# Kernel optimization log

Measured on AMD Instinct MI355X. Metric: run time of the kernel, lower is better.

## Reference

```python
import jax, jax.numpy as jnp
import numpy as np

LMBDA = 0.01
GAMMA = 0.5  # resolvant_gamma


def get_mask(evals_x, evals_y, gamma):
    # Standard DPFM resolvant mask, vectorized over batch.
    # evals_x, evals_y: [B, K] nonnegative eigenvalues.
    scale = jnp.maximum(evals_x.max(-1), evals_y.max(-1))[:, None]  # per-batch scaling
    e1 = (evals_x / scale) ** gamma  # [B, K] -> columns of D
    e2 = (evals_y / scale) ** gamma  # [B, K] -> rows of D
    denom = e1[:, None, :] ** 2 + e2[:, :, None] ** 2  # [B, K, K]
    M_re = (e2[:, :, None] - e1[:, None, :]) / denom
    M_im = 1.0 / denom
    return M_re ** 2 + M_im ** 2  # [B, K, K]


def setup_inputs() -> dict:
    key = jax.random.key(0)
    kA, kB, kx, ky = jax.random.split(key, 4)
    Bsz, K, C = 8, 200, 352
    A = jax.random.normal(kA, (Bsz, K, C), dtype=jnp.float32)
    B = jax.random.normal(kB, (Bsz, K, C), dtype=jnp.float32)
    evals_x = jax.random.uniform(kx, (Bsz, K), dtype=jnp.float32)
    evals_y = jax.random.uniform(ky, (Bsz, K), dtype=jnp.float32)
    return {"A": A, "B": B, "evals_x": evals_x, "evals_y": evals_y}


def reference(A, B, evals_x, evals_y):
    # A, B: [Bsz, K, C]; evals_*: [Bsz, K]
    D = get_mask(evals_x, evals_y, GAMMA)  # [Bsz, K, K]
    A_t = jnp.swapaxes(A, 1, 2)            # [Bsz, C, K]
    A_A_t = jnp.matmul(A, A_t)             # [Bsz, K, K]
    B_A_t = jnp.matmul(B, A_t)             # [Bsz, K, K]
    K = A.shape[1]
    eye = jnp.eye(K, dtype=A.dtype)
    # mats[b, i] = A_A_t[b] + lmbda * diag(D[b, i, :])  -> [Bsz, K, K, K]
    mats = A_A_t[:, None, :, :] + LMBDA * (D[..., None] * eye)
    rhs = B_A_t[..., None]                 # [Bsz, K, K, 1] (row i of B_A_t as column)
    # Solve each regularized system; rows of Cxy are the solutions.
    Cxy = jnp.linalg.solve(mats, rhs)[..., 0]  # [Bsz, K, K]
    return Cxy
```

## Files before the change

kernel.cpp:

```cpp
#include <hip/hip_runtime.h>
#include <math.h>

#define KD 200
#define CD 352
#define NITER 28
#define LMB 0.01f

__device__ __forceinline__ float4 ld4(const float* p) { return *(const float4*)p; }
__device__ __forceinline__ void st4(float* p, float4 v) { *(float4*)p = v; }
__device__ __forceinline__ float rdlane(float v, int lane) {
    return __int_as_float(__builtin_amdgcn_readlane(__float_as_int(v), lane));
}

__global__ __launch_bounds__(256) void gemm_gr_kernel(
    const float* __restrict__ A, const float* __restrict__ B,
    float* __restrict__ G, float* __restrict__ R)
{
    __shared__ __align__(16) float Ms[16][72];
    __shared__ __align__(16) float Ns[16][72];
    const int tid = threadIdx.x;
    const int z = blockIdx.z;
    const int b = z >> 1, which = z & 1;
    const float* __restrict__ Xb = (which ? B : A) + (size_t)b * KD * CD;
    const float* __restrict__ Ab = A + (size_t)b * KD * CD;
    float* __restrict__ O = (which ? R : G) + (size_t)b * KD * KD;
    const int tileM = blockIdx.y * 64;
    const int tileN = blockIdx.x * 64;

    const int lm = tid >> 2;
    const int kq = (tid & 3) * 4;
    const int rowM = min(tileM + lm, KD - 1);
    const int rowN = min(tileN + lm, KD - 1);
    const float* __restrict__ Xrow = Xb + (size_t)rowM * CD;
    const float* __restrict__ Arow = Ab + (size_t)rowN * CD;

    const int ty = tid >> 4, tx = tid & 15;
    const int m0 = ty * 4, n0 = tx * 4;

    float acc[4][4] = {};
    for (int kk = 0; kk < CD; kk += 16) {
        const float4 vx = ld4(Xrow + kk + kq);
        const float4 va = ld4(Arow + kk + kq);
        __syncthreads();
        Ms[kq + 0][lm] = vx.x; Ms[kq + 1][lm] = vx.y;
        Ms[kq + 2][lm] = vx.z; Ms[kq + 3][lm] = vx.w;
        Ns[kq + 0][lm] = va.x; Ns[kq + 1][lm] = va.y;
        Ns[kq + 2][lm] = va.z; Ns[kq + 3][lm] = va.w;
        __syncthreads();
        #pragma unroll
        for (int k = 0; k < 16; ++k) {
            const float4 am = ld4(&Ms[k][m0]);
            const float4 an = ld4(&Ns[k][n0]);
            acc[0][0] = fmaf(am.x, an.x, acc[0][0]);
            acc[0][1] = fmaf(am.x, an.y, acc[0][1]);
            acc[0][2] = fmaf(am.x, an.z, acc[0][2]);
            acc[0][3] = fmaf(am.x, an.w, acc[0][3]);
            acc[1][0] = fmaf(am.y, an.x, acc[1][0]);
            acc[1][1] = fmaf(am.y, an.y, acc[1][1]);
            acc[1][2] = fmaf(am.y, an.z, acc[1][2]);
            acc[1][3] = fmaf(am.y, an.w, acc[1][3]);
            acc[2][0] = fmaf(am.z, an.x, acc[2][0]);
            acc[2][1] = fmaf(am.z, an.y, acc[2][1]);
            acc[2][2] = fmaf(am.z, an.z, acc[2][2]);
            acc[2][3] = fmaf(am.z, an.w, acc[2][3]);
            acc[3][0] = fmaf(am.w, an.x, acc[3][0]);
            acc[3][1] = fmaf(am.w, an.y, acc[3][1]);
            acc[3][2] = fmaf(am.w, an.z, acc[3][2]);
            acc[3][3] = fmaf(am.w, an.w, acc[3][3]);
        }
    }
    const int gn = tileN + n0;
    if (gn < KD) {
        #pragma unroll
        for (int i = 0; i < 4; ++i) {
            const int gm = tileM + m0 + i;
            if (gm < KD)
                st4(&O[(size_t)gm * KD + gn],
                    make_float4(acc[i][0], acc[i][1], acc[i][2], acc[i][3]));
        }
    }
}

__global__ __launch_bounds__(512) void cg_kernel(
    const float* __restrict__ G, const float* __restrict__ R,
    const float* __restrict__ ex, const float* __restrict__ ey,
    float* __restrict__ out)
{
    __shared__ __align__(16) float P[KD * 8];
    __shared__ __align__(16) float PART[8 * KD * 8];
    __shared__ float WP1[8][8];
    __shared__ float WP2[8][8];
    __shared__ float red8[8];

    const int tid = threadIdx.x;
    const int w = tid >> 6, l = tid & 63;
    const int blk = blockIdx.x;
    const int b = blk / 25;
    const int i0 = (blk - b * 25) * 8;
    const int bK = b * KD;
    const float* __restrict__ Gb = G + (size_t)b * KD * KD;

    float mxv = 0.f;
    if (tid < KD) mxv = fmaxf(ex[bK + tid], ey[bK + tid]);
    #pragma unroll
    for (int off = 32; off > 0; off >>= 1)
        mxv = fmaxf(mxv, __shfl_down(mxv, off, 64));
    if (l == 0) red8[w] = mxv;
    __syncthreads();
    float scale = red8[0];
    #pragma unroll
    for (int wv = 1; wv < 8; ++wv) scale = fmaxf(scale, red8[wv]);
    const float inv_scale = 1.0f / scale;

    const bool mact = (l < 50);
    const int gcol = mact ? l : 49;

    float4 g0[8];
    {
        const float* __restrict__ gp = Gb + (size_t)(w * 8) * KD + gcol;
        #pragma unroll
        for (int dc = 0; dc < 8; ++dc) {
            g0[dc] = make_float4(gp[0], gp[50], gp[100], gp[150]);
            gp += KD;
        }
    }

    const bool stid = tid < 400;
    const int r = tid >> 1, sq = tid & 1;
    float lam[4], dinv[4], rr[4], xx[4], pp[4], rz4[4];
    if (stid) {
        const float exj = ex[bK + r] * inv_scale;
        const float e1 = sqrtf(exj);
        const float gdiag = Gb[(size_t)r * KD + r];
        const float* __restrict__ Rb = R + (size_t)(bK + i0 + sq * 4) * KD + r;
        #pragma unroll
        for (int j = 0; j < 4; ++j) {
            const float eyi = ey[bK + i0 + sq * 4 + j] * inv_scale;
            const float e2 = sqrtf(eyi);
            const float dn = exj + eyi;
            const float re = e2 - e1;
            lam[j] = LMB * ((re * re + 1.f) / (dn * dn));
            dinv[j] = 1.f / (gdiag + lam[j]);
            rr[j] = Rb[(size_t)j * KD];
            pp[j] = rr[j] * dinv[j];
            xx[j] = 0.f;
        }
        st4(&P[r * 8 + sq * 4], make_float4(pp[0], pp[1], pp[2], pp[3]));
    }
    {
        float vg[4];
        #pragma unroll
        for (int j = 0; j < 4; ++j) vg[j] = stid ? rr[j] * pp[j] : 0.f;
        #pragma unroll
        for (int off = 2; off < 64; off <<= 1)
            #pragma unroll
            for (int j = 0; j < 4; ++j) vg[j] += __shfl_xor(vg[j], off, 64);
        if (l < 2) {
            #pragma unroll
            for (int j = 0; j < 4; ++j) WP1[w][l * 4 + j] = vg[j];
        }
    }
    __syncthreads();
    if (stid) {
        #pragma unroll
        for (int j = 0; j < 4; ++j) {
            float s = 0.f;
            #pragma unroll
            for (int w8 = 0; w8 < 8; ++w8) s += WP1[w8][sq * 4 + j];
            rz4[j] = s;
        }
    }

    for (int k = 0; k < NITER; ++k) {
        __syncthreads();

        float acc[4][8];
        #pragma unroll
        for (int j = 0; j < 4; ++j)
            #pragma unroll
            for (int s = 0; s < 8; ++s) acc[j][s] = 0.f;

        {
            const float pv = P[w * 64 + l];
            #pragma unroll
            for (int dc = 0; dc < 8; ++dc) {
                const float4 g = g0[dc];
                #pragma unroll
                for (int s = 0; s < 8; ++s) {
                    const float ps = rdlane(pv, dc * 8 + s);
                    acc[0][s] = fmaf(g.x, ps, acc[0][s]);
                    acc[1][s] = fmaf(g.y, ps, acc[1][s]);
                    acc[2][s] = fmaf(g.z, ps, acc[2][s]);
                    acc[3][s] = fmaf(g.w, ps, acc[3][s]);
                }
            }
        }
        #pragma unroll
        for (int t = 1; t < 3; ++t) {
            const int jc = w + t * 8;
            const float pv = P[jc * 64 + l];
            const float* __restrict__ gp = Gb + (size_t)(jc * 8) * KD + gcol;
            #pragma unroll
            for (int dc = 0; dc < 8; ++dc) {
                const float g0v = gp[0];
                const float g1v = gp[50];
                const float g2v = gp[100];
                const float g3v = gp[150];
                #pragma unroll
                for (int s = 0; s < 8; ++s) {
                    const float ps = rdlane(pv, dc * 8 + s);
                    acc[0][s] = fmaf(g0v, ps, acc[0][s]);
                    acc[1][s] = fmaf(g1v, ps, acc[1][s]);
                    acc[2][s] = fmaf(g2v, ps, acc[2][s]);
                    acc[3][s] = fmaf(g3v, ps, acc[3][s]);
                }
                gp += KD;
            }
        }
        {
            const float pv24 = P[24 * 64 + l];
            const float* __restrict__ gp24 = Gb + (size_t)(192 + w) * KD + gcol;
            const float g0v = gp24[0];
            const float g1v = gp24[50];
            const float g2v = gp24[100];
            const float g3v = gp24[150];
            #pragma unroll
            for (int s = 0; s < 8; ++s) {
                const float ps = rdlane(pv24, w * 8 + s);
                acc[0][s] = fmaf(g0v, ps, acc[0][s]);
                acc[1][s] = fmaf(g1v, ps, acc[1][s]);
                acc[2][s] = fmaf(g2v, ps, acc[2][s]);
                acc[3][s] = fmaf(g3v, ps, acc[3][s]);
            }
        }
        if (mact) {
            #pragma unroll
            for (int j = 0; j < 4; ++j) {
                float* pw = &PART[w * (KD * 8) + (50 * j + l) * 8];
                st4(pw,     make_float4(acc[j][0], acc[j][1], acc[j][2], acc[j][3]));
                st4(pw + 4, make_float4(acc[j][4], acc[j][5], acc[j][6], acc[j][7]));
            }
        }
        __syncthreads();

        float qq[4], vq[4];
        if (stid) {
            float4 sum = make_float4(0.f, 0.f, 0.f, 0.f);
            #pragma unroll
            for (int w8 = 0; w8 < 8; ++w8) {
                const float4 f = ld4(&PART[w8 * (KD * 8) + r * 8 + sq * 4]);
                sum.x += f.x; sum.y += f.y; sum.z += f.z; sum.w += f.w;
            }
            qq[0] = fmaf(lam[0], pp[0], sum.x);
            qq[1] = fmaf(lam[1], pp[1], sum.y);
            qq[2] = fmaf(lam[2], pp[2], sum.z);
            qq[3] = fmaf(lam[3], pp[3], sum.w);
            #pragma unroll
            for (int j = 0; j < 4; ++j) vq[j] = pp[j] * qq[j];
        } else {
            #pragma unroll
            for (int j = 0; j < 4; ++j) { qq[j] = 0.f; vq[j] = 0.f; }
        }
        #pragma unroll
        for (int off = 2; off < 64; off <<= 1)
            #pragma unroll
            for (int j = 0; j < 4; ++j) vq[j] += __shfl_xor(vq[j], off, 64);
        if (l < 2) {
            #pragma unroll
            for (int j = 0; j < 4; ++j) WP1[w][l * 4 + j] = vq[j];
        }
        __syncthreads();

        float vr[4];
        if (stid) {
            #pragma unroll
            for (int j = 0; j < 4; ++j) {
                float pq = 0.f;
                #pragma unroll
                for (int w8 = 0; w8 < 8; ++w8) pq += WP1[w8][sq * 4 + j];
                const float alpha = rz4[j] / pq;
                xx[j] = fmaf(alpha, pp[j], xx[j]);
                rr[j] = fmaf(-alpha, qq[j], rr[j]);
                vr[j] = rr[j] * rr[j] * dinv[j];
            }
        } else {
            #pragma unroll
            for (int j = 0; j < 4; ++j) vr[j] = 0.f;
        }
        #pragma unroll
        for (int off = 2; off < 64; off <<= 1)
            #pragma unroll
            for (int j = 0; j < 4; ++j) vr[j] += __shfl_xor(vr[j], off, 64);
        if (l < 2) {
            #pragma unroll
            for (int j = 0; j < 4; ++j) WP2[w][l * 4 + j] = vr[j];
        }
        __syncthreads();

        if (stid) {
            #pragma unroll
            for (int j = 0; j < 4; ++j) {
                float rzn = 0.f;
                #pragma unroll
                for (int w8 = 0; w8 < 8; ++w8) rzn += WP2[w8][sq * 4 + j];
                const float beta = rzn / rz4[j];
                rz4[j] = rzn;
                pp[j] = fmaf(beta, pp[j], rr[j] * dinv[j]);
            }
            st4(&P[r * 8 + sq * 4], make_float4(pp[0], pp[1], pp[2], pp[3]));
        }
    }

    if (stid) {
        float* __restrict__ Ob = out + (size_t)(bK + i0 + sq * 4) * KD + r;
        #pragma unroll
        for (int j = 0; j < 4; ++j)
            Ob[(size_t)j * KD] = xx[j];
    }
}

extern "C" void kernel_launch(void* const* d_in, const int* in_sizes, int n_in,
                              void* d_out, int out_size, void* d_ws, size_t ws_size,
                              hipStream_t stream) {
    const float* A  = (const float*)d_in[0];
    const float* B  = (const float*)d_in[1];
    const float* ex = (const float*)d_in[2];
    const float* ey = (const float*)d_in[3];
    float* out = (float*)d_out;

    float* G = (float*)d_ws;
    float* R = G + 8 * KD * KD;

    dim3 grid1(4, 4, 16);
    gemm_gr_kernel<<<grid1, 256, 0, stream>>>(A, B, G, R);

    cg_kernel<<<200, 512, 0, stream>>>(G, R, ex, ey, out);
}
```

Measured before the change: 239.8 us.

## Fuse lambda term and p·q reduction into matvec phase, drop one barrier, cut iterations

Each CG iteration now computes the diagonal lambda*p term and the p·q dot product right after the G·p partial matvec. That per-wave reduction is combined with the PART write, which removes one __syncthreads and one reduction round per iteration. Register-cached G rows for the first chunk are dropped, so all of G is reloaded from global or L2 each iteration, which may raise register headroom but adds memory traffic. The iteration count also drops from 28 to 24, which risks accuracy of the iterative solve.

```diff
diff --git a/kernel.cpp b/kernel.cpp
--- a/kernel.cpp
+++ b/kernel.cpp
@@ -3,7 +3,7 @@
 
 #define KD 200
 #define CD 352
-#define NITER 28
+#define NITER 24
 #define LMB 0.01f
 
 __device__ __forceinline__ float4 ld4(const float* p) { return *(const float4*)p; }
@@ -87,9 +87,10 @@
     float* __restrict__ out)
 {
     __shared__ __align__(16) float P[KD * 8];
+    __shared__ __align__(16) float LAM[KD * 8];
     __shared__ __align__(16) float PART[8 * KD * 8];
-    __shared__ float WP1[8][8];
-    __shared__ float WP2[8][8];
+    __shared__ __align__(16) float WP1[8][8];
+    __shared__ __align__(16) float WP2[8][8];
     __shared__ float red8[8];
 
     const int tid = threadIdx.x;
@@ -115,16 +116,6 @@
     const bool mact = (l < 50);
     const int gcol = mact ? l : 49;
 
-    float4 g0[8];
-    {
-        const float* __restrict__ gp = Gb + (size_t)(w * 8) * KD + gcol;
-        #pragma unroll
-        for (int dc = 0; dc < 8; ++dc) {
-            g0[dc] = make_float4(gp[0], gp[50], gp[100], gp[150]);
-            gp += KD;
-        }
-    }
-
     const bool stid = tid < 400;
     const int r = tid >> 1, sq = tid & 1;
     float lam[4], dinv[4], rr[4], xx[4], pp[4], rz4[4];
@@ -146,6 +137,7 @@
             xx[j] = 0.f;
         }
         st4(&P[r * 8 + sq * 4], make_float4(pp[0], pp[1], pp[2], pp[3]));
+        st4(&LAM[r * 8 + sq * 4], make_float4(lam[0], lam[1], lam[2], lam[3]));
     }
     {
         float vg[4];
@@ -157,7 +149,7 @@
             for (int j = 0; j < 4; ++j) vg[j] += __shfl_xor(vg[j], off, 64);
         if (l < 2) {
             #pragma unroll
-            for (int j = 0; j < 4; ++j) WP1[w][l * 4 + j] = vg[j];
+            for (int j = 0; j < 4; ++j) WP2[w][l * 4 + j] = vg[j];
         }
     }
     __syncthreads();
@@ -166,7 +158,7 @@
         for (int j = 0; j < 4; ++j) {
             float s = 0.f;
             #pragma unroll
-            for (int w8 = 0; w8 < 8; ++w8) s += WP1[w8][sq * 4 + j];
+            for (int w8 = 0; w8 < 8; ++w8) s += WP2[w8][sq * 4 + j];
             rz4[j] = s;
         }
     }
@@ -180,23 +172,8 @@
             #pragma unroll
             for (int s = 0; s < 8; ++s) acc[j][s] = 0.f;
 
-        {
-            const float pv = P[w * 64 + l];
-            #pragma unroll
-            for (int dc = 0; dc < 8; ++dc) {
-                const float4 g = g0[dc];
-                #pragma unroll
-                for (int s = 0; s < 8; ++s) {
-                    const float ps = rdlane(pv, dc * 8 + s);
-                    acc[0][s] = fmaf(g.x, ps, acc[0][s]);
-                    acc[1][s] = fmaf(g.y, ps, acc[1][s]);
-                    acc[2][s] = fmaf(g.z, ps, acc[2][s]);
-                    acc[3][s] = fmaf(g.w, ps, acc[3][s]);
-                }
-            }
-        }
-        #pragma unroll
-        for (int t = 1; t < 3; ++t) {
+        #pragma unroll
+        for (int t = 0; t < 3; ++t) {
             const int jc = w + t * 8;
             const float pv = P[jc * 64 + l];
             const float* __restrict__ gp = Gb + (size_t)(jc * 8) * KD + gcol;
@@ -233,6 +210,53 @@
                 acc[3][s] = fmaf(g3v, ps, acc[3][s]);
             }
         }
+
+        if (w == 0 && mact) {
+            #pragma unroll
+            for (int j = 0; j < 4; ++j) {
+                const int row = l + 50 * j;
+                const float4 la0 = ld4(&LAM[row * 8]);
+                const float4 la1 = ld4(&LAM[row * 8 + 4]);
+                const float4 pa0 = ld4(&P[row * 8]);
+                const float4 pa1 = ld4(&P[row * 8 + 4]);
+                acc[j][0] = fmaf(la0.x, pa0.x, acc[j][0]);
+                acc[j][1] = fmaf(la0.y, pa0.y, acc[j][1]);
+                acc[j][2] = fmaf(la0.z, pa0.z, acc[j][2]);
+                acc[j][3] = fmaf(la0.w, pa0.w, acc[j][3]);
+                acc[j][4] = fmaf(la1.x, pa1.x, acc[j][4]);
+                acc[j][5] = fmaf(la1.y, pa1.y, acc[j][5]);
+                acc[j][6] = fmaf(la1.z, pa1.z, acc[j][6]);
+                acc[j][7] = fmaf(la1.w, pa1.w, acc[j][7]);
+            }
+        }
+
+        float vqp[8];
+        #pragma unroll
+        for (int s = 0; s < 8; ++s) vqp[s] = 0.f;
+        if (mact) {
+            #pragma unroll
+            for (int j = 0; j < 4; ++j) {
+                const int row = l + 50 * j;
+                const float4 pa0 = ld4(&P[row * 8]);
+                const float4 pa1 = ld4(&P[row * 8 + 4]);
+                vqp[0] = fmaf(pa0.x, acc[j][0], vqp[0]);
+                vqp[1] = fmaf(pa0.y, acc[j][1], vqp[1]);
+                vqp[2] = fmaf(pa0.z, acc[j][2], vqp[2]);
+                vqp[3] = fmaf(pa0.w, acc[j][3], vqp[3]);
+                vqp[4] = fmaf(pa1.x, acc[j][4], vqp[4]);
+                vqp[5] = fmaf(pa1.y, acc[j][5], vqp[5]);
+                vqp[6] = fmaf(pa1.z, acc[j][6], vqp[6]);
+                vqp[7] = fmaf(pa1.w, acc[j][7], vqp[7]);
+            }
+        }
+        #pragma unroll
+        for (int off = 1; off < 64; off <<= 1)
+            #pragma unroll
+            for (int s = 0; s < 8; ++s) vqp[s] += __shfl_xor(vqp[s], off, 64);
+        if (l == 0) {
+            st4(&WP1[w][0], make_float4(vqp[0], vqp[1], vqp[2], vqp[3]));
+            st4(&WP1[w][4], make_float4(vqp[4], vqp[5], vqp[6], vqp[7]));
+        }
         if (mact) {
             #pragma unroll
             for (int j = 0; j < 4; ++j) {
@@ -243,7 +267,7 @@
         }
         __syncthreads();
 
-        float qq[4], vq[4];
+        float vr[4];
         if (stid) {
             float4 sum = make_float4(0.f, 0.f, 0.f, 0.f);
             #pragma unroll
@@ -251,28 +275,7 @@
                 const float4 f = ld4(&PART[w8 * (KD * 8) + r * 8 + sq * 4]);
                 sum.x += f.x; sum.y += f.y; sum.z += f.z; sum.w += f.w;
             }
-            qq[0] = fmaf(lam[0], pp[0], sum.x);
-            qq[1] = fmaf(lam[1], pp[1], sum.y);
-            qq[2] = fmaf(lam[2], pp[2], sum.z);
-            qq[3] = fmaf(lam[3], pp[3], sum.w);
-            #pragma unroll
-            for (int j = 0; j < 4; ++j) vq[j] = pp[j] * qq[j];
-        } else {
-            #pragma unroll
-            for (int j = 0; j < 4; ++j) { qq[j] = 0.f; vq[j] = 0.f; }
-        }
-        #pragma unroll
-        for (int off = 2; off < 64; off <<= 1)
-            #pragma unroll
-            for (int j = 0; j < 4; ++j) vq[j] += __shfl_xor(vq[j], off, 64);
-        if (l < 2) {
-            #pragma unroll
-            for (int j = 0; j < 4; ++j) WP1[w][l * 4 + j] = vq[j];
-        }
-        __syncthreads();
-
-        float vr[4];
-        if (stid) {
+            const float qv[4] = {sum.x, sum.y, sum.z, sum.w};
             #pragma unroll
             for (int j = 0; j < 4; ++j) {
                 float pq = 0.f;
@@ -280,7 +283,7 @@
                 for (int w8 = 0; w8 < 8; ++w8) pq += WP1[w8][sq * 4 + j];
                 const float alpha = rz4[j] / pq;
                 xx[j] = fmaf(alpha, pp[j], xx[j]);
-                rr[j] = fmaf(-alpha, qq[j], rr[j]);
+                rr[j] = fmaf(-alpha, qv[j], rr[j]);
                 vr[j] = rr[j] * rr[j] * dinv[j];
             }
         } else {
```

After: 266.7 us. +11.2%, slower.
